# Performance work log

Hardware: AMD Instinct MI355X
Metric: run time of the kernel (lower is better)

Reference implementation:

```python
import jax, jax.numpy as jnp
import numpy as np

NEG = -100000000.0  # NOT_POSSIBLE_TRANSITION
B, T, F, NT = 64, 512, 1024, 50
H = NT + 2  # +2 for start/stop tags
START, STOP = H - 2, H - 1


def setup_inputs() -> dict:
    key = jax.random.key(0)
    k0, k1, k2, k3 = jax.random.split(key, 4)
    features = jax.random.normal(k0, (B, T, F), jnp.float32)
    tags = jax.random.randint(k1, (B, T), 0, NT)
    masks = jnp.ones((B, T), jnp.float32)
    W = jax.random.normal(k2, (H, F), jnp.float32) * 0.02  # nn.Linear weight
    b = jnp.zeros((H,), jnp.float32)                        # nn.Linear bias
    transition = jax.random.normal(k3, (H, H), jnp.float32)
    transition = transition.at[START, :].set(NEG).at[:, STOP].set(NEG)
    return dict(features=features, W=W, b=b, transition=transition,
                masks=masks, tags=tags)


def _forward_algorithm(emit, masks, transition):
    # emit: [B,T,H], masks: [B,T]
    b_, _, h = emit.shape
    init = jnp.full((b_, h), NEG, emit.dtype).at[:, START].set(0.0)

    def step(scores, xs):
        emit_t, mask_t = xs  # [B,H], [B]
        # score_t[b, i] = logsumexp_j(scores[b,j] + transition[i,j] + emit_t[b,i])
        s = scores[:, None, :] + transition[None, :, :] + emit_t[:, :, None]
        s = jax.nn.logsumexp(s, axis=-1)
        m = mask_t[:, None]
        scores = s * m + scores * (1.0 - m)
        return scores, None

    scores, _ = jax.lax.scan(step, init, (emit.transpose(1, 0, 2), masks.T))
    return jax.nn.logsumexp(scores + transition[STOP], axis=-1)  # [B]


def _gold_score(emit, tags, masks, transition):
    b_ = emit.shape[0]
    emit_sc = jnp.take_along_axis(emit, tags[:, :, None], axis=2)[:, :, 0]  # [B,T]
    start = jnp.full((b_, 1), START, tags.dtype)
    tags_ext = jnp.concatenate([start, tags], axis=1)  # [B,T+1]
    trans_sc = transition[tags_ext[:, 1:], tags_ext[:, :-1]]  # [B,T]
    last_pos = masks.sum(axis=1).astype(jnp.int32)  # index into tags_ext
    last_tag = jnp.take_along_axis(tags_ext, last_pos[:, None], axis=1)[:, 0]
    last_score = transition[STOP, last_tag]
    return ((trans_sc + emit_sc) * masks).sum(axis=1) + last_score  # [B]


def reference(features, W, b, transition, masks, tags):
    emit = features @ W.T + b  # [B,T,H]
    fwd = _forward_algorithm(emit, masks, transition)
    gold = _gold_score(emit, tags, masks, transition)
    return (fwd - gold).mean()  # CRF NLL loss (scalar)


if __name__ == "__main__":
    print(reference(**setup_inputs()))
```

## Files before the change

kernel.cpp:

```cpp
#include <hip/hip_runtime.h>
#include <hip/hip_bf16.h>
#include <math.h>


#define NEGV   (-100000000.0f)
#define BB     64
#define TT     512
#define FF     1024
#define HH     52
#define HP     64
#define S_START 50
#define S_STOP  51
#define NCH    16
#define CLEN   (TT / NCH)

typedef __bf16 bf16x8 __attribute__((ext_vector_type(8)));
typedef __bf16 bf16x4 __attribute__((ext_vector_type(4)));
typedef float  f32x4  __attribute__((ext_vector_type(4)));

#define WS_EMIT   0u
#define WS_CHUNK  8388608u
#define WS_WBF    25165824u
#define WS_GOLD   25296896u
#define WS_CEXP   25297152u

__global__ __launch_bounds__(256) void k_prep(const float* __restrict__ W,
                                              __bf16* __restrict__ wbf) {
  int n = blockIdx.x;
  for (int k = threadIdx.x; k < FF; k += 256) {
    float v = (n < HH) ? W[n * FF + k] : 0.0f;
    wbf[n * FF + k] = (__bf16)v;
  }
}

__global__ __launch_bounds__(256) void k_emit(const float* __restrict__ feat,
                                              const __bf16* __restrict__ wbf,
                                              const float* __restrict__ bias,
                                              float* __restrict__ emit) {
  const int tid = threadIdx.x;
  const int wv = tid >> 6;
  const int l  = tid & 63;
  const int lm = l & 15;
  const int q  = l >> 4;
  const size_t row0 = (size_t)blockIdx.x * 64;
  const float* fr = feat + (row0 + wv * 16 + lm) * FF;

  float bn[4];
#pragma unroll
  for (int nt = 0; nt < 4; ++nt) {
    int n = nt * 16 + lm;
    bn[nt] = (n < HH) ? bias[n] : 0.0f;
  }

  f32x4 acc[4] = {};

  f32x4 xa[2][2];
#pragma unroll
  for (int kk = 0; kk < 2; ++kk)
#pragma unroll
    for (int h = 0; h < 2; ++h)
      xa[kk][h] = *(const f32x4*)(fr + kk * 32 + q * 8 + h * 4);

  for (int kc = 0; kc < 16; ++kc) {
    bf16x8 af[2];
#pragma unroll
    for (int kk = 0; kk < 2; ++kk)
#pragma unroll
      for (int j = 0; j < 4; ++j) {
        af[kk][j]     = (__bf16)xa[kk][0][j];
        af[kk][4 + j] = (__bf16)xa[kk][1][j];
      }
    f32x4 xn[2][2];
    if (kc < 15) {
      const float* nf = fr + (kc + 1) * 64;
#pragma unroll
      for (int kk = 0; kk < 2; ++kk)
#pragma unroll
        for (int h = 0; h < 2; ++h)
          xn[kk][h] = *(const f32x4*)(nf + kk * 32 + q * 8 + h * 4);
    }
    const int k0 = kc * 64;
#pragma unroll
    for (int kk = 0; kk < 2; ++kk)
#pragma unroll
      for (int nt = 0; nt < 4; ++nt) {
        bf16x8 bfr = *(const bf16x8*)(wbf + (size_t)(nt * 16 + lm) * FF + k0 + kk * 32 + q * 8);
        acc[nt] = __builtin_amdgcn_mfma_f32_16x16x32_bf16(af[kk], bfr, acc[nt], 0, 0, 0);
      }
#pragma unroll
    for (int kk = 0; kk < 2; ++kk)
#pragma unroll
      for (int h = 0; h < 2; ++h)
        xa[kk][h] = xn[kk][h];
  }

#pragma unroll
  for (int nt = 0; nt < 4; ++nt) {
#pragma unroll
    for (int rr = 0; rr < 4; ++rr) {
      size_t m = row0 + wv * 16 + q * 4 + rr;
      emit[m * HP + nt * 16 + lm] = acc[nt][rr] + bn[nt];
    }
  }
}

__global__ __launch_bounds__(256) void k_gold(const float* __restrict__ emit,
                                              const int* __restrict__ tags,
                                              const float* __restrict__ masks,
                                              const float* __restrict__ trans,
                                              float* __restrict__ gold) {
  const int b = blockIdx.x;
  const int tid = threadIdx.x;
  float acc = 0.f, msum = 0.f;
  for (int t = tid; t < TT; t += 256) {
    int tg = tags[b * TT + t];
    int pv = (t == 0) ? S_START : tags[b * TT + t - 1];
    float m = masks[b * TT + t];
    float e = emit[((size_t)b * TT + t) * HP + tg];
    float tr = trans[tg * HH + pv];
    acc += (e + tr) * m;
    msum += m;
  }
#pragma unroll
  for (int d = 32; d > 0; d >>= 1) {
    acc += __shfl_xor(acc, d);
    msum += __shfl_xor(msum, d);
  }
  __shared__ float ra[4], rm[4];
  if ((tid & 63) == 0) { ra[tid >> 6] = acc; rm[tid >> 6] = msum; }
  __syncthreads();
  if (tid == 0) {
    float tot = ra[0] + ra[1] + ra[2] + ra[3];
    float ms  = rm[0] + rm[1] + rm[2] + rm[3];
    int lp = (int)(ms + 0.5f);
    int lt = (lp == 0) ? S_START : tags[b * TT + lp - 1];
    gold[b] = tot + trans[S_STOP * HH + lt];
  }
}

__global__ __launch_bounds__(256, 1) void k_chunks(const float* __restrict__ emit,
                                                   const float* __restrict__ trans,
                                                   const float* __restrict__ masks,
                                                   float* __restrict__ chunks,
                                                   float* __restrict__ cexp) {
  const int tid = threadIdx.x;
  const int wv = tid >> 6;
  const int l  = tid & 63;
  const int lm = l & 15;
  const int q  = l >> 4;
  const int chunk = blockIdx.x * 4 + wv;
  const int b = chunk >> 4, c = chunk & 15;

  __shared__ __align__(16) __bf16 PTall[4][64 * 72];
  __bf16* pt = PTall[wv];

  bf16x8 afrag[4][2];
#pragma unroll
  for (int mt = 0; mt < 4; ++mt)
#pragma unroll
    for (int kk = 0; kk < 2; ++kk)
#pragma unroll
      for (int j = 0; j < 8; ++j) {
        int m = mt * 16 + lm, k = kk * 32 + q * 8 + j;
        float tv = (k >= HH) ? NEGV : ((m >= HH) ? 0.0f : trans[m * HH + k]);
        afrag[mt][kk][j] = (__bf16)__expf(tv);
      }

  for (int idx = l; idx < 4096; idx += 64) {
    int n = idx >> 6, mm = idx & 63;
    pt[n * 72 + mm] = (__bf16)((n == mm) ? 1.0f : 0.0f);
  }

  const float* eb = emit + ((size_t)(b * TT + c * CLEN)) * HP;
  const float* mb = masks + b * TT + c * CLEN;

  f32x4 ep[4];
#pragma unroll
  for (int mt = 0; mt < 4; ++mt) ep[mt] = *(const f32x4*)(eb + mt * 16 + q * 4);
  float mpf = mb[0];

  int eacc = 0, rpend = 0;
  const float LOG2E = 1.4426950408889634f;

  for (int t = 0; t < CLEN; ++t) {
    f32x4 ec[4];
#pragma unroll
    for (int mt = 0; mt < 4; ++mt) ec[mt] = ep[mt];
    float mcur = mpf;
    int tn = (t + 1 < CLEN) ? t + 1 : t;
#pragma unroll
    for (int mt = 0; mt < 4; ++mt)
      ep[mt] = *(const f32x4*)(eb + (size_t)tn * HP + mt * 16 + q * 4);
    mpf = mb[tn];

    if (mcur != 0.0f) {
      float sh = (float)(7 + rpend);
      eacc += 7 + rpend;
      rpend = 0;
      float s[4][4];
#pragma unroll
      for (int mt = 0; mt < 4; ++mt)
#pragma unroll
        for (int rr = 0; rr < 4; ++rr)
          s[mt][rr] = __builtin_amdgcn_exp2f(fmaf(ec[mt][rr], LOG2E, -sh));

      bf16x8 bfr[2][4];
#pragma unroll
      for (int kk = 0; kk < 2; ++kk)
#pragma unroll
        for (int nt = 0; nt < 4; ++nt)
          bfr[kk][nt] = *(const bf16x8*)&pt[(nt * 16 + lm) * 72 + kk * 32 + q * 8];

      const bool trk = ((t & 7) == 7) && (t != CLEN - 1);
      float lmax = 0.0f;
      f32x4 zero = {};
#pragma unroll
      for (int mt = 0; mt < 4; ++mt) {
#pragma unroll
        for (int nt = 0; nt < 4; ++nt) {
          f32x4 a = __builtin_amdgcn_mfma_f32_16x16x32_bf16(afrag[mt][0], bfr[0][nt], zero, 0, 0, 0);
          a = __builtin_amdgcn_mfma_f32_16x16x32_bf16(afrag[mt][1], bfr[1][nt], a, 0, 0, 0);
          bf16x4 w4;
#pragma unroll
          for (int rr = 0; rr < 4; ++rr) {
            float v = a[rr] * s[mt][rr];
            if (trk) lmax = fmaxf(lmax, v);
            w4[rr] = (__bf16)v;
          }
          *(bf16x4*)&pt[(nt * 16 + lm) * 72 + mt * 16 + q * 4] = w4;
        }
      }
      if (trk) {
#pragma unroll
        for (int d = 1; d < 64; d <<= 1) lmax = fmaxf(lmax, __shfl_xor(lmax, d));
        rpend = ilogbf(lmax);
      }
    }
  }

  for (int idx = l; idx < 4096; idx += 64) {
    int jj = idx >> 8, i = (idx >> 2) & 63, jr = idx & 3;
    chunks[(size_t)chunk * 4096 + idx] = (float)pt[(jj * 4 + jr) * 72 + i];
  }
  if (l == 0) cexp[chunk] = (float)eacc;
}

__global__ __launch_bounds__(64) void k_combine(const float* __restrict__ chunks,
                                                const float* __restrict__ cexp,
                                                const float* __restrict__ trans,
                                                const float* __restrict__ gold,
                                                float* __restrict__ out) {
  const int b = blockIdx.x;
  const int l = threadIdx.x;
  __shared__ float vsh[64];
  float v = (l == S_START) ? 1.0f : 0.0f;
  float esum = 0.0f;
  const float LN2 = 0.6931471805599453f;

  for (int cc = 0; cc < NCH; ++cc) {
    vsh[l] = v;
    __syncthreads();
    const f32x4* M = (const f32x4*)(chunks + ((size_t)(b * NCH + cc)) * 4096);
    f32x4 u4 = {};
#pragma unroll
    for (int jj = 0; jj < 16; ++jj) {
      f32x4 m4 = M[jj * 64 + l];
      const float* vj = &vsh[jj * 4];
      u4[0] += m4[0] * vj[0];
      u4[1] += m4[1] * vj[1];
      u4[2] += m4[2] * vj[2];
      u4[3] += m4[3] * vj[3];
    }
    float u = (u4[0] + u4[1]) + (u4[2] + u4[3]);
    esum += cexp[b * NCH + cc] * LN2;
    float mxx = u;
#pragma unroll
    for (int d = 1; d < 64; d <<= 1) mxx = fmaxf(mxx, __shfl_xor(mxx, d));
    if (mxx > 0.0f) {
      int ee = ilogbf(mxx);
      u = ldexpf(u, -ee);
      esum += (float)ee * LN2;
    }
    v = u;
    __syncthreads();
  }

  float ts = (l < HH) ? trans[S_STOP * HH + l] : NEGV;
  float contrib = v * __expf(ts);
#pragma unroll
  for (int d = 1; d < 64; d <<= 1) contrib += __shfl_xor(contrib, d);
  if (l == 0) {
    float fwd = __logf(contrib) + esum;
    atomicAdd(out, (fwd - gold[b]) * (1.0f / 64.0f));
  }
}

extern "C" void kernel_launch(void* const* d_in, const int* in_sizes, int n_in,
                              void* d_out, int out_size, void* d_ws, size_t ws_size,
                              hipStream_t stream) {
  (void)in_sizes; (void)n_in; (void)out_size; (void)ws_size;
  const float* feat  = (const float*)d_in[0];
  const float* W     = (const float*)d_in[1];
  const float* bias  = (const float*)d_in[2];
  const float* trans = (const float*)d_in[3];
  const float* masks = (const float*)d_in[4];
  const int*   tags  = (const int*)d_in[5];

  char* ws = (char*)d_ws;
  float*  emit   = (float*)(ws + WS_EMIT);
  float*  chunks = (float*)(ws + WS_CHUNK);
  __bf16* wbf    = (__bf16*)(ws + WS_WBF);
  float*  gold   = (float*)(ws + WS_GOLD);
  float*  cexp   = (float*)(ws + WS_CEXP);

  hipMemsetAsync(d_out, 0, sizeof(float), stream);
  k_prep<<<HP, 256, 0, stream>>>(W, wbf);
  k_emit<<<(BB * TT) / 64, 256, 0, stream>>>(feat, wbf, bias, emit);
  k_gold<<<BB, 256, 0, stream>>>(emit, tags, masks, trans, gold);
  k_chunks<<<(BB * NCH) / 4, 256, 0, stream>>>(emit, trans, masks, chunks, cexp);
  k_combine<<<BB, 64, 0, stream>>>(chunks, cexp, trans, gold, (float*)d_out);
}
```

Before: 280.9 us.

## Fuse emission GEMM and gold score into the chunked forward-scan kernel

Each wave of the chunk-scan kernel now computes its own 32x64 emission tile from the features via bf16 MFMA and keeps it in shared memory, so the emit buffer no longer round-trips through global memory. The gold score is also accumulated there with atomics, and the final-tag term moves into the combine kernel. The combine kernel gains register double-buffering of the chunk matrices. In exchange, only 256 blocks of one-wave-per-chunk now do the whole feature GEMM with lower parallelism, and shared-memory use per block grows.

```diff
diff --git a/kernel.cpp b/kernel.cpp
--- a/kernel.cpp
+++ b/kernel.cpp
@@ -18,131 +18,31 @@
 typedef __bf16 bf16x4 __attribute__((ext_vector_type(4)));
 typedef float  f32x4  __attribute__((ext_vector_type(4)));
 
-#define WS_EMIT   0u
-#define WS_CHUNK  8388608u
-#define WS_WBF    25165824u
-#define WS_GOLD   25296896u
-#define WS_CEXP   25297152u
+#define WS_CHUNK  0u
+#define WS_WBF    16777216u
+#define WS_GOLD   16908288u
+#define WS_CEXP   16908544u
 
 __global__ __launch_bounds__(256) void k_prep(const float* __restrict__ W,
-                                              __bf16* __restrict__ wbf) {
+                                              __bf16* __restrict__ wbf,
+                                              float* __restrict__ gold) {
   int n = blockIdx.x;
+  if (n == 0 && threadIdx.x < BB) gold[threadIdx.x] = 0.0f;
   for (int k = threadIdx.x; k < FF; k += 256) {
     float v = (n < HH) ? W[n * FF + k] : 0.0f;
     wbf[n * FF + k] = (__bf16)v;
   }
 }
 
-__global__ __launch_bounds__(256) void k_emit(const float* __restrict__ feat,
-                                              const __bf16* __restrict__ wbf,
-                                              const float* __restrict__ bias,
-                                              float* __restrict__ emit) {
-  const int tid = threadIdx.x;
-  const int wv = tid >> 6;
-  const int l  = tid & 63;
-  const int lm = l & 15;
-  const int q  = l >> 4;
-  const size_t row0 = (size_t)blockIdx.x * 64;
-  const float* fr = feat + (row0 + wv * 16 + lm) * FF;
-
-  float bn[4];
-#pragma unroll
-  for (int nt = 0; nt < 4; ++nt) {
-    int n = nt * 16 + lm;
-    bn[nt] = (n < HH) ? bias[n] : 0.0f;
-  }
-
-  f32x4 acc[4] = {};
-
-  f32x4 xa[2][2];
-#pragma unroll
-  for (int kk = 0; kk < 2; ++kk)
-#pragma unroll
-    for (int h = 0; h < 2; ++h)
-      xa[kk][h] = *(const f32x4*)(fr + kk * 32 + q * 8 + h * 4);
-
-  for (int kc = 0; kc < 16; ++kc) {
-    bf16x8 af[2];
-#pragma unroll
-    for (int kk = 0; kk < 2; ++kk)
-#pragma unroll
-      for (int j = 0; j < 4; ++j) {
-        af[kk][j]     = (__bf16)xa[kk][0][j];
-        af[kk][4 + j] = (__bf16)xa[kk][1][j];
-      }
-    f32x4 xn[2][2];
-    if (kc < 15) {
-      const float* nf = fr + (kc + 1) * 64;
-#pragma unroll
-      for (int kk = 0; kk < 2; ++kk)
-#pragma unroll
-        for (int h = 0; h < 2; ++h)
-          xn[kk][h] = *(const f32x4*)(nf + kk * 32 + q * 8 + h * 4);
-    }
-    const int k0 = kc * 64;
-#pragma unroll
-    for (int kk = 0; kk < 2; ++kk)
-#pragma unroll
-      for (int nt = 0; nt < 4; ++nt) {
-        bf16x8 bfr = *(const bf16x8*)(wbf + (size_t)(nt * 16 + lm) * FF + k0 + kk * 32 + q * 8);
-        acc[nt] = __builtin_amdgcn_mfma_f32_16x16x32_bf16(af[kk], bfr, acc[nt], 0, 0, 0);
-      }
-#pragma unroll
-    for (int kk = 0; kk < 2; ++kk)
-#pragma unroll
-      for (int h = 0; h < 2; ++h)
-        xa[kk][h] = xn[kk][h];
-  }
-
-#pragma unroll
-  for (int nt = 0; nt < 4; ++nt) {
-#pragma unroll
-    for (int rr = 0; rr < 4; ++rr) {
-      size_t m = row0 + wv * 16 + q * 4 + rr;
-      emit[m * HP + nt * 16 + lm] = acc[nt][rr] + bn[nt];
-    }
-  }
-}
-
-__global__ __launch_bounds__(256) void k_gold(const float* __restrict__ emit,
-                                              const int* __restrict__ tags,
-                                              const float* __restrict__ masks,
-                                              const float* __restrict__ trans,
-                                              float* __restrict__ gold) {
-  const int b = blockIdx.x;
-  const int tid = threadIdx.x;
-  float acc = 0.f, msum = 0.f;
-  for (int t = tid; t < TT; t += 256) {
-    int tg = tags[b * TT + t];
-    int pv = (t == 0) ? S_START : tags[b * TT + t - 1];
-    float m = masks[b * TT + t];
-    float e = emit[((size_t)b * TT + t) * HP + tg];
-    float tr = trans[tg * HH + pv];
-    acc += (e + tr) * m;
-    msum += m;
-  }
-#pragma unroll
-  for (int d = 32; d > 0; d >>= 1) {
-    acc += __shfl_xor(acc, d);
-    msum += __shfl_xor(msum, d);
-  }
-  __shared__ float ra[4], rm[4];
-  if ((tid & 63) == 0) { ra[tid >> 6] = acc; rm[tid >> 6] = msum; }
-  __syncthreads();
-  if (tid == 0) {
-    float tot = ra[0] + ra[1] + ra[2] + ra[3];
-    float ms  = rm[0] + rm[1] + rm[2] + rm[3];
-    int lp = (int)(ms + 0.5f);
-    int lt = (lp == 0) ? S_START : tags[b * TT + lp - 1];
-    gold[b] = tot + trans[S_STOP * HH + lt];
-  }
-}
-
-__global__ __launch_bounds__(256, 1) void k_chunks(const float* __restrict__ emit,
-                                                   const float* __restrict__ trans,
-                                                   const float* __restrict__ masks,
-                                                   float* __restrict__ chunks,
-                                                   float* __restrict__ cexp) {
+__global__ __launch_bounds__(256, 1) void k_scan(const float* __restrict__ feat,
+                                                 const __bf16* __restrict__ wbf,
+                                                 const float* __restrict__ bias,
+                                                 const float* __restrict__ trans,
+                                                 const float* __restrict__ masks,
+                                                 const int* __restrict__ tags,
+                                                 float* __restrict__ chunks,
+                                                 float* __restrict__ cexp,
+                                                 float* __restrict__ gold) {
   const int tid = threadIdx.x;
   const int wv = tid >> 6;
   const int l  = tid & 63;
@@ -152,7 +52,88 @@
   const int b = chunk >> 4, c = chunk & 15;
 
   __shared__ __align__(16) __bf16 PTall[4][64 * 72];
+  __shared__ __align__(16) float  Eall[4][CLEN * 64];
   __bf16* pt = PTall[wv];
+  float*  el = Eall[wv];
+
+  const float* fbase = feat + ((size_t)(b * TT + c * CLEN)) * FF;
+
+  f32x4 apre[2][2][2];
+#pragma unroll
+  for (int s = 0; s < 2; ++s)
+#pragma unroll
+    for (int mt2 = 0; mt2 < 2; ++mt2)
+#pragma unroll
+      for (int h = 0; h < 2; ++h)
+        apre[s][mt2][h] = *(const f32x4*)(fbase + (size_t)(mt2 * 16 + lm) * FF + s * 32 + q * 8 + h * 4);
+
+  bf16x8 bcur[4];
+#pragma unroll
+  for (int nt = 0; nt < 4; ++nt)
+    bcur[nt] = *(const bf16x8*)(wbf + (size_t)(nt * 16 + lm) * FF + q * 8);
+
+  f32x4 acc[2][4] = {};
+
+#pragma unroll
+  for (int kt = 0; kt < 32; ++kt) {
+    const int st = kt & 1;
+    bf16x8 af[2];
+#pragma unroll
+    for (int mt2 = 0; mt2 < 2; ++mt2)
+#pragma unroll
+      for (int j = 0; j < 4; ++j) {
+        af[mt2][j]     = (__bf16)apre[st][mt2][0][j];
+        af[mt2][4 + j] = (__bf16)apre[st][mt2][1][j];
+      }
+    if (kt + 2 < 32) {
+      const float* fa = fbase + (kt + 2) * 32 + q * 8;
+#pragma unroll
+      for (int mt2 = 0; mt2 < 2; ++mt2)
+#pragma unroll
+        for (int h = 0; h < 2; ++h)
+          apre[st][mt2][h] = *(const f32x4*)(fa + (size_t)(mt2 * 16 + lm) * FF + h * 4);
+    }
+    bf16x8 bnx[4];
+    if (kt + 1 < 32) {
+#pragma unroll
+      for (int nt = 0; nt < 4; ++nt)
+        bnx[nt] = *(const bf16x8*)(wbf + (size_t)(nt * 16 + lm) * FF + (kt + 1) * 32 + q * 8);
+    }
+#pragma unroll
+    for (int mt2 = 0; mt2 < 2; ++mt2)
+#pragma unroll
+      for (int nt = 0; nt < 4; ++nt)
+        acc[mt2][nt] = __builtin_amdgcn_mfma_f32_16x16x32_bf16(af[mt2], bcur[nt], acc[mt2][nt], 0, 0, 0);
+    if (kt + 1 < 32) {
+#pragma unroll
+      for (int nt = 0; nt < 4; ++nt) bcur[nt] = bnx[nt];
+    }
+  }
+
+#pragma unroll
+  for (int nt = 0; nt < 4; ++nt) {
+    int n = nt * 16 + lm;
+    float bn = (n < HH) ? bias[n] : 0.0f;
+#pragma unroll
+    for (int mt2 = 0; mt2 < 2; ++mt2)
+#pragma unroll
+      for (int rr = 0; rr < 4; ++rr)
+        el[(mt2 * 16 + q * 4 + rr) * 64 + n] = acc[mt2][nt][rr] + bn;
+  }
+
+  float mreg = (l < CLEN) ? masks[b * TT + c * CLEN + l] : 1.0f;
+  int cur = (l < CLEN) ? tags[b * TT + c * CLEN + l] : 0;
+  int prev = __shfl_up(cur, 1);
+  if (l == 0) prev = (c == 0) ? S_START : tags[b * TT + c * CLEN - 1];
+  float gp = 0.0f;
+  if (l < CLEN) {
+    float e  = el[l * 64 + cur];
+    float tr = trans[cur * HH + prev];
+    gp = (e + tr) * mreg;
+  }
+#pragma unroll
+  for (int d = 1; d < 64; d <<= 1) gp += __shfl_xor(gp, d);
+  if (l == 0) atomicAdd(&gold[b], gp);
 
   bf16x8 afrag[4][2];
 #pragma unroll
@@ -171,38 +152,23 @@
     pt[n * 72 + mm] = (__bf16)((n == mm) ? 1.0f : 0.0f);
   }
 
-  const float* eb = emit + ((size_t)(b * TT + c * CLEN)) * HP;
-  const float* mb = masks + b * TT + c * CLEN;
-
-  f32x4 ep[4];
-#pragma unroll
-  for (int mt = 0; mt < 4; ++mt) ep[mt] = *(const f32x4*)(eb + mt * 16 + q * 4);
-  float mpf = mb[0];
-
   int eacc = 0, rpend = 0;
   const float LOG2E = 1.4426950408889634f;
 
   for (int t = 0; t < CLEN; ++t) {
-    f32x4 ec[4];
-#pragma unroll
-    for (int mt = 0; mt < 4; ++mt) ec[mt] = ep[mt];
-    float mcur = mpf;
-    int tn = (t + 1 < CLEN) ? t + 1 : t;
-#pragma unroll
-    for (int mt = 0; mt < 4; ++mt)
-      ep[mt] = *(const f32x4*)(eb + (size_t)tn * HP + mt * 16 + q * 4);
-    mpf = mb[tn];
-
+    float mcur = __shfl(mreg, t);
     if (mcur != 0.0f) {
       float sh = (float)(7 + rpend);
       eacc += 7 + rpend;
       rpend = 0;
       float s[4][4];
 #pragma unroll
-      for (int mt = 0; mt < 4; ++mt)
+      for (int mt = 0; mt < 4; ++mt) {
+        f32x4 em = *(const f32x4*)&el[t * 64 + mt * 16 + q * 4];
 #pragma unroll
         for (int rr = 0; rr < 4; ++rr)
-          s[mt][rr] = __builtin_amdgcn_exp2f(fmaf(ec[mt][rr], LOG2E, -sh));
+          s[mt][rr] = __builtin_amdgcn_exp2f(fmaf(em[rr], LOG2E, -sh));
+      }
 
       bf16x8 bfr[2][4];
 #pragma unroll
@@ -248,6 +214,8 @@
 __global__ __launch_bounds__(64) void k_combine(const float* __restrict__ chunks,
                                                 const float* __restrict__ cexp,
                                                 const float* __restrict__ trans,
+                                                const float* __restrict__ masks,
+                                                const int* __restrict__ tags,
                                                 const float* __restrict__ gold,
                                                 float* __restrict__ out) {
   const int b = blockIdx.x;
@@ -257,14 +225,29 @@
   float esum = 0.0f;
   const float LN2 = 0.6931471805599453f;
 
+  float msum = 0.0f;
+  for (int t = l; t < TT; t += 64) msum += masks[b * TT + t];
+
+  f32x4 mb[2][16];
+  {
+    const f32x4* M = (const f32x4*)(chunks + ((size_t)(b * NCH)) * 4096);
+#pragma unroll
+    for (int jj = 0; jj < 16; ++jj) mb[0][jj] = M[jj * 64 + l];
+  }
+
+#pragma unroll
   for (int cc = 0; cc < NCH; ++cc) {
     vsh[l] = v;
     __syncthreads();
-    const f32x4* M = (const f32x4*)(chunks + ((size_t)(b * NCH + cc)) * 4096);
+    if (cc + 1 < NCH) {
+      const f32x4* Mn = (const f32x4*)(chunks + ((size_t)(b * NCH + cc + 1)) * 4096);
+#pragma unroll
+      for (int jj = 0; jj < 16; ++jj) mb[(cc + 1) & 1][jj] = Mn[jj * 64 + l];
+    }
     f32x4 u4 = {};
 #pragma unroll
     for (int jj = 0; jj < 16; ++jj) {
-      f32x4 m4 = M[jj * 64 + l];
+      f32x4 m4 = mb[cc & 1][jj];
       const float* vj = &vsh[jj * 4];
       u4[0] += m4[0] * vj[0];
       u4[1] += m4[1] * vj[1];
@@ -288,10 +271,16 @@
   float ts = (l < HH) ? trans[S_STOP * HH + l] : NEGV;
   float contrib = v * __expf(ts);
 #pragma unroll
-  for (int d = 1; d < 64; d <<= 1) contrib += __shfl_xor(contrib, d);
+  for (int d = 1; d < 64; d <<= 1) {
+    contrib += __shfl_xor(contrib, d);
+    msum += __shfl_xor(msum, d);
+  }
   if (l == 0) {
+    int lp = (int)(msum + 0.5f);
+    int lt = (lp == 0) ? S_START : tags[b * TT + lp - 1];
+    float goldb = gold[b] + trans[S_STOP * HH + lt];
     float fwd = __logf(contrib) + esum;
-    atomicAdd(out, (fwd - gold[b]) * (1.0f / 64.0f));
+    atomicAdd(out, (fwd - goldb) * (1.0f / 64.0f));
   }
 }
 
@@ -307,16 +296,14 @@
   const int*   tags  = (const int*)d_in[5];
 
   char* ws = (char*)d_ws;
-  float*  emit   = (float*)(ws + WS_EMIT);
   float*  chunks = (float*)(ws + WS_CHUNK);
   __bf16* wbf    = (__bf16*)(ws + WS_WBF);
   float*  gold   = (float*)(ws + WS_GOLD);
   float*  cexp   = (float*)(ws + WS_CEXP);
 
   hipMemsetAsync(d_out, 0, sizeof(float), stream);
-  k_prep<<<HP, 256, 0, stream>>>(W, wbf);
-  k_emit<<<(BB * TT) / 64, 256, 0, stream>>>(feat, wbf, bias, emit);
-  k_gold<<<BB, 256, 0, stream>>>(emit, tags, masks, trans, gold);
-  k_chunks<<<(BB * NCH) / 4, 256, 0, stream>>>(emit, trans, masks, chunks, cexp);
-  k_combine<<<BB, 64, 0, stream>>>(chunks, cexp, trans, gold, (float*)d_out);
+  k_prep<<<HP, 256, 0, stream>>>(W, wbf, gold);
+  k_scan<<<(BB * NCH) / 4, 256, 0, stream>>>(feat, wbf, bias, trans, masks, tags,
+                                             chunks, cexp, gold);
+  k_combine<<<BB, 64, 0, stream>>>(chunks, cexp, trans, masks, tags, gold, (float*)d_out);
 }
```

Result: faster. 270.5 us (-3.7%).
